# Performance work log

Hardware: AMD Instinct MI355X
Metric: run time of the kernel (lower is better)

Reference implementation:

```python
import jax, jax.numpy as jnp
import numpy as np

H, C_K, C_Q = 4, 512, 512


def setup_inputs() -> dict:
    key = jax.random.key(0)
    ks = jax.random.split(key, 6)
    s = 1.0 / np.sqrt(512.0)
    return {
        "x_k": jax.random.normal(ks[0], (4096, 512), jnp.float32),
        "x_q": jax.random.normal(ks[1], (4096, 512), jnp.float32),
        "k_w": jax.random.normal(ks[2], (H * C_K, 512), jnp.float32) * s,
        "q_w": jax.random.normal(ks[3], (H * C_Q, 512), jnp.float32) * s,
        "attn_w": jax.random.normal(ks[4], (H, C_K, C_Q), jnp.float32) * s,
        "proj_w": jax.random.normal(ks[5], (C_K, C_Q), jnp.float32) * s,
    }


def reference(x_k, x_q, k_w, q_w, attn_w, proj_w):
    # Project keys/queries and split into heads: [H, N, c]
    xk = (x_k @ k_w.T).reshape(-1, H, C_K).transpose(1, 0, 2)
    xq = (x_q @ q_w.T).reshape(-1, H, C_Q).transpose(1, 0, 2)
    # Bilinear scores: alphas[h, n, m] = xk[h,n,:] @ attn_w[h] @ xq[h,m,:]
    alphas = jnp.einsum("hnk,hkq,hmq->hnm", xk, attn_w, xq)
    # key-side update
    alpha_ks = jax.nn.softmax(alphas, axis=2)                 # [H, Nk, Nq]
    alpha_k_agg = jnp.mean(jnp.einsum("hnm,hmq->hnq", alpha_ks, xq), axis=0)
    x_k_update = alpha_k_agg @ proj_w.T                       # [Nk, C_K]
    # query-side update (bidirectional)
    alpha_qs = jax.nn.softmax(alphas.transpose(0, 2, 1), axis=2)  # [H, Nq, Nk]
    alpha_q_agg = jnp.mean(jnp.einsum("hmn,hnk->hmk", alpha_qs, xk), axis=0)
    x_q_update = alpha_q_agg @ proj_w                         # [Nq, C_Q]
    return x_k + x_k_update, x_q + x_q_update
```

## Files before the change

### kernel.cpp

```cpp
#include <hip/hip_runtime.h>
#include <stdint.h>

#define DEVI __device__ __forceinline__

typedef unsigned short u16;
typedef unsigned int u32;
typedef __attribute__((ext_vector_type(4))) unsigned short u16x4;
typedef __attribute__((ext_vector_type(8))) unsigned short u16x8;
typedef __attribute__((ext_vector_type(4))) float f32x4;
typedef __attribute__((ext_vector_type(8))) _Float16 f16x8;

static constexpr int NT = 4096;
static constexpr int D  = 512;
static constexpr int NH = 4;
static constexpr int KS = 4;

DEVI u16 f2h(float f) {
  _Float16 h = (_Float16)f;
  union { _Float16 h; u16 u; } v; v.h = h;
  return v.u;
}
DEVI float h2f(u16 u) {
  union { u16 u; _Float16 h; } v; v.u = u;
  return (float)v.h;
}

DEVI u32 enc_ord(float f) {
  u32 u = __float_as_uint(f);
  return (u & 0x80000000u) ? ~u : (u | 0x80000000u);
}
DEVI float dec_ord(u32 k) {
  u32 u = (k & 0x80000000u) ? (k ^ 0x80000000u) : ~k;
  return __uint_as_float(u);
}

DEVI void gld_lds16(const u16* g, u16* l) {
  __builtin_amdgcn_global_load_lds((const __attribute__((address_space(1))) void*)g,
                                   (__attribute__((address_space(3))) void*)l, 16, 0, 0);
}

enum { OUT_F32 = 0, OUT_F16 = 2, OUT_RES = 3, OUT_SMAX = 4, OUT_F16T = 5 };

template<int OUT>
__global__ __launch_bounds__(256)
void gemm_bt(const u16* __restrict__ A, int lda, size_t zsA,
             const u16* __restrict__ B, int ldb, size_t zsB,
             void* __restrict__ Cp, int ldc, size_t zsC,
             const float* __restrict__ res, const float* __restrict__ res2, int K,
             u32* __restrict__ rmg, u32* __restrict__ cmg,
             u16* __restrict__ STp, int ldct, size_t zsT)
{
  constexpr bool DOT = (OUT == OUT_SMAX || OUT == OUT_F16T);
  __shared__ u16 As[128 * 32];
  __shared__ u16 Bs[128 * 32];
  __shared__ u32 rmaxs[128], cmaxs[128];
  __shared__ u16 Tt[DOT ? 128 * 72 : 8];
  A += blockIdx.z * zsA;
  B += blockIdx.z * zsB;
  const float* resz = (OUT == OUT_RES && blockIdx.z) ? res2 : res;
  const int tid = threadIdx.x;
  const int lane = tid & 63, w = tid >> 6;
  const int wr = w >> 1, wc = w & 1;
  const int m0 = blockIdx.y * 128, n0 = blockIdx.x * 128;

  if (OUT == OUT_SMAX && tid < 128) { rmaxs[tid] = 0u; cmaxs[tid] = 0u; }

  f32x4 acc[4][4] = {};

  for (int k0 = 0; k0 < K; k0 += 32) {
    __syncthreads();
#pragma unroll
    for (int p = 0; p < 2; ++p) {
      int id = p * 256 + tid;
      int row = id >> 2, q = id & 3;
      gld_lds16(A + (size_t)(m0 + row) * lda + k0 + q * 8, As + id * 8);
      gld_lds16(B + (size_t)(n0 + row) * ldb + k0 + q * 8, Bs + id * 8);
    }
    __syncthreads();
    f16x8 af[4], bfv[4];
#pragma unroll
    for (int i = 0; i < 4; ++i)
      af[i] = *(const f16x8*)(As + (wr * 64 + i * 16 + (lane & 15)) * 32 + (lane >> 4) * 8);
#pragma unroll
    for (int i = 0; i < 4; ++i)
      bfv[i] = *(const f16x8*)(Bs + (wc * 64 + i * 16 + (lane & 15)) * 32 + (lane >> 4) * 8);
#pragma unroll
    for (int i = 0; i < 4; ++i)
#pragma unroll
      for (int j = 0; j < 4; ++j)
        acc[i][j] = __builtin_amdgcn_mfma_f32_16x16x32_f16(af[i], bfv[j], acc[i][j], 0, 0, 0);
  }

  if (!DOT) {
#pragma unroll
    for (int i = 0; i < 4; ++i) {
      int rl0 = wr * 64 + i * 16 + (lane >> 4) * 4;
#pragma unroll
      for (int j = 0; j < 4; ++j) {
        int c = n0 + wc * 64 + j * 16 + (lane & 15);
#pragma unroll
        for (int e = 0; e < 4; ++e) {
          size_t idx = blockIdx.z * zsC + (size_t)(m0 + rl0 + e) * ldc + c;
          float v = acc[i][j][e];
          if (OUT == OUT_F32) ((float*)Cp)[idx] = v;
          if (OUT == OUT_F16) ((u16*)Cp)[idx] = f2h(v);
          if (OUT == OUT_RES) ((float*)Cp)[idx] = resz[(size_t)(m0 + rl0 + e) * ldc + c] + v;
        }
      }
    }
  }

  if (OUT == OUT_SMAX) {
#pragma unroll
    for (int i = 0; i < 4; ++i) {
      int rl0 = wr * 64 + i * 16 + (lane >> 4) * 4;
#pragma unroll
      for (int e = 0; e < 4; ++e) {
        float m = fmaxf(fmaxf(acc[i][0][e], acc[i][1][e]), fmaxf(acc[i][2][e], acc[i][3][e]));
        atomicMax(&rmaxs[rl0 + e], enc_ord(m));
      }
    }
#pragma unroll
    for (int j = 0; j < 4; ++j) {
      float m = -3e38f;
#pragma unroll
      for (int i = 0; i < 4; ++i)
#pragma unroll
        for (int e = 0; e < 4; ++e) m = fmaxf(m, acc[i][j][e]);
      atomicMax(&cmaxs[wc * 64 + j * 16 + (lane & 15)], enc_ord(m));
    }
    __syncthreads();
    if (tid < 128) {
      atomicMax(rmg + m0 + tid, rmaxs[tid]);
      atomicMax(cmg + n0 + tid, cmaxs[tid]);
    }
  }

  if (DOT) {
#pragma unroll
    for (int chalf = 0; chalf < 2; ++chalf) {
      __syncthreads();
      if (wc == chalf) {
#pragma unroll
        for (int i = 0; i < 4; ++i) {
          int rl0 = wr * 64 + i * 16 + (lane >> 4) * 4;
#pragma unroll
          for (int j = 0; j < 4; ++j) {
            int c63 = j * 16 + (lane & 15);
#pragma unroll
            for (int e = 0; e < 4; ++e)
              Tt[(rl0 + e) * 72 + c63] = f2h(acc[i][j][e]);
          }
        }
      }
      __syncthreads();
#pragma unroll
      for (int q = 0; q < 4; ++q) {
        int id2 = q * 256 + tid;
        int r = id2 >> 3, c8 = (id2 & 7) * 8;
        u16x8 v = *(const u16x8*)&Tt[r * 72 + c8];
        *(u16x8*)((u16*)Cp + blockIdx.z * zsC + (size_t)(m0 + r) * ldc + n0 + chalf * 64 + c8) = v;
      }
    }
#pragma unroll
    for (int half = 0; half < 2; ++half) {
      __syncthreads();
      if (wr == half) {
#pragma unroll
        for (int i = 0; i < 4; ++i) {
          int rl = i * 16 + (lane >> 4) * 4;
#pragma unroll
          for (int j = 0; j < 4; ++j) {
            int cl = wc * 64 + j * 16 + (lane & 15);
            u16x4 v;
            v[0] = f2h(acc[i][j][0]); v[1] = f2h(acc[i][j][1]);
            v[2] = f2h(acc[i][j][2]); v[3] = f2h(acc[i][j][3]);
            *(u16x4*)&Tt[cl * 72 + rl] = v;
          }
        }
      }
      __syncthreads();
#pragma unroll
      for (int q = 0; q < 4; ++q) {
        int id2 = q * 256 + tid;
        int c = id2 >> 3, mm = (id2 & 7) * 8;
        u16x8 v = *(const u16x8*)&Tt[c * 72 + mm];
        *(u16x8*)(STp + blockIdx.z * zsT + (size_t)(n0 + c) * ldct + m0 + half * 64 + mm) = v;
      }
    }
  }
}

__global__ __launch_bounds__(256)
void pv(const u16* __restrict__ Sarg, const u32* __restrict__ mx_u,
        const u16* __restrict__ B,
        u16* __restrict__ part, float* __restrict__ lpart, int Ksl)
{
  __shared__ u16 As[64 * 40];
  __shared__ u16 Bs[128 * 32];
  __shared__ float ps[4][64];
  const int tid = threadIdx.x;
  const int lane = tid & 63, w = tid >> 6;
  const int wr = w >> 1, wc = w & 1;
  const int m0 = blockIdx.y * 64, n0 = blockIdx.x * 128;
  const int kb = blockIdx.z * Ksl;

  const int rA = tid >> 2, kc = (tid & 3) * 8;
  const float mxA = dec_ord(mx_u[m0 + rA]);
  const u16* S0 = Sarg + (size_t)(m0 + rA) * NT + kb + kc;

  f32x4 acc[2][4] = {};
  float sacc = 0.f;

  f16x8 sv0 = *(const f16x8*)S0;

  for (int k0 = 0; k0 < Ksl; k0 += 32) {
    __syncthreads();
#pragma unroll
    for (int p = 0; p < 2; ++p) {
      int id = p * 256 + tid;
      int row = id >> 2, q = id & 3;
      gld_lds16(B + (size_t)(n0 + row) * NT + kb + k0 + q * 8, Bs + id * 8);
    }
    f16x8 nx0;
    if (k0 + 32 < Ksl) nx0 = *(const f16x8*)(S0 + k0 + 32);
    {
      u16x8 pk;
      float rs = 0.f;
#pragma unroll
      for (int j = 0; j < 8; ++j) {
        float e = __expf((float)sv0[j] - mxA);
        rs += e; pk[j] = f2h(e);
      }
      *(u16x8*)(As + rA * 40 + kc) = pk;
      sacc += rs;
    }
    __syncthreads();
    f16x8 af[2], bfv[4];
#pragma unroll
    for (int i = 0; i < 2; ++i)
      af[i] = *(const f16x8*)(As + (wr * 32 + i * 16 + (lane & 15)) * 40 + (lane >> 4) * 8);
#pragma unroll
    for (int j = 0; j < 4; ++j)
      bfv[j] = *(const f16x8*)(Bs + (wc * 64 + j * 16 + (lane & 15)) * 32 + (lane >> 4) * 8);
#pragma unroll
    for (int i = 0; i < 2; ++i)
#pragma unroll
      for (int j = 0; j < 4; ++j)
        acc[i][j] = __builtin_amdgcn_mfma_f32_16x16x32_f16(af[i], bfv[j], acc[i][j], 0, 0, 0);
    sv0 = nx0;
  }

  u16* out = part + (size_t)blockIdx.z * NT * D;
#pragma unroll
  for (int i = 0; i < 2; ++i) {
    int r0 = m0 + wr * 32 + i * 16 + (lane >> 4) * 4;
#pragma unroll
    for (int j = 0; j < 4; ++j) {
      int c = n0 + wc * 64 + j * 16 + (lane & 15);
#pragma unroll
      for (int e = 0; e < 4; ++e)
        out[(size_t)(r0 + e) * D + c] = f2h(acc[i][j][e]);
    }
  }

  __syncthreads();
  ps[tid & 3][tid >> 2] = sacc;
  __syncthreads();
  if (blockIdx.x == 0 && tid < 64) {
    lpart[(size_t)blockIdx.z * NT + m0 + tid] =
        ps[0][tid] + ps[1][tid] + ps[2][tid] + ps[3][tid];
  }
}

__global__ __launch_bounds__(256)
void reduce2(const u16* __restrict__ pk, const float* __restrict__ lk,
             const u16* __restrict__ pq, const float* __restrict__ lq,
             u16* __restrict__ a0h, u16* __restrict__ a1h)
{
  const size_t i = ((size_t)blockIdx.x * 256 + threadIdx.x) * 4;
  const int m = (int)(i >> 9);
  const size_t zs = (size_t)NT * D;
  float Lk = 0.f, Lq = 0.f;
#pragma unroll
  for (int z = 0; z < KS; ++z) { Lk += lk[(size_t)z * NT + m]; Lq += lq[(size_t)z * NT + m]; }
  float s0 = 0.f, s1 = 0.f, s2 = 0.f, s3 = 0.f;
#pragma unroll
  for (int z = 0; z < KS; ++z) {
    u16x4 v = *(const u16x4*)(pk + z * zs + i);
    s0 += h2f(v[0]); s1 += h2f(v[1]); s2 += h2f(v[2]); s3 += h2f(v[3]);
  }
  float ck = 0.25f / Lk;
  u16x4 a = *(const u16x4*)(a0h + i);
  u16x4 na;
  na[0] = f2h(h2f(a[0]) + s0 * ck); na[1] = f2h(h2f(a[1]) + s1 * ck);
  na[2] = f2h(h2f(a[2]) + s2 * ck); na[3] = f2h(h2f(a[3]) + s3 * ck);
  *(u16x4*)(a0h + i) = na;
  s0 = s1 = s2 = s3 = 0.f;
#pragma unroll
  for (int z = 0; z < KS; ++z) {
    u16x4 v = *(const u16x4*)(pq + z * zs + i);
    s0 += h2f(v[0]); s1 += h2f(v[1]); s2 += h2f(v[2]); s3 += h2f(v[3]);
  }
  float cq = 0.25f / Lq;
  u16x4 b = *(const u16x4*)(a1h + i);
  u16x4 nb;
  nb[0] = f2h(h2f(b[0]) + s0 * cq); nb[1] = f2h(h2f(b[1]) + s1 * cq);
  nb[2] = f2h(h2f(b[2]) + s2 * cq); nb[3] = f2h(h2f(b[3]) + s3 * cq);
  *(u16x4*)(a1h + i) = nb;
}

__global__ __launch_bounds__(256)
void cast_f32_f16(const float* __restrict__ in, u16* __restrict__ out, int n)
{
  int i = (blockIdx.x * 256 + threadIdx.x) * 8;
  if (i >= n) return;
  f32x4 a = *(const f32x4*)(in + i), b = *(const f32x4*)(in + i + 4);
  u16x8 s;
  s[0] = f2h(a[0]); s[1] = f2h(a[1]); s[2] = f2h(a[2]); s[3] = f2h(a[3]);
  s[4] = f2h(b[0]); s[5] = f2h(b[1]); s[6] = f2h(b[2]); s[7] = f2h(b[3]);
  *(u16x8*)(out + i) = s;
}

__global__ __launch_bounds__(256)
void transpose_cast_f32(const float* __restrict__ in, int ldi,
                        u16* __restrict__ out, int ldo)
{
  __shared__ u16 t[64][72];
  int r0 = blockIdx.x * 64, c0 = blockIdx.y * 64;
  int t8 = threadIdx.x & 7, rr = threadIdx.x >> 3;
#pragma unroll
  for (int p = 0; p < 2; ++p) {
    int r = rr + p * 32;
    const float* src = in + (size_t)(r0 + r) * ldi + c0 + t8 * 8;
    f32x4 a = *(const f32x4*)src, b = *(const f32x4*)(src + 4);
    u16x8 s;
    s[0] = f2h(a[0]); s[1] = f2h(a[1]); s[2] = f2h(a[2]); s[3] = f2h(a[3]);
    s[4] = f2h(b[0]); s[5] = f2h(b[1]); s[6] = f2h(b[2]); s[7] = f2h(b[3]);
    *(u16x8*)&t[r][t8 * 8] = s;
  }
  __syncthreads();
#pragma unroll
  for (int p = 0; p < 2; ++p) {
    int c = rr + p * 32;
    u16x8 s;
#pragma unroll
    for (int j = 0; j < 8; ++j) s[j] = t[t8 * 8 + j][c];
    *(u16x8*)(out + (size_t)(c0 + c) * ldo + r0 + t8 * 8) = s;
  }
}

extern "C" void kernel_launch(void* const* d_in, const int* in_sizes, int n_in,
                              void* d_out, int out_size, void* d_ws, size_t ws_size,
                              hipStream_t stream)
{
  const float* x_k    = (const float*)d_in[0];
  const float* x_q    = (const float*)d_in[1];
  const float* k_w    = (const float*)d_in[2];
  const float* q_w    = (const float*)d_in[3];
  const float* attn_w = (const float*)d_in[4];
  const float* proj_w = (const float*)d_in[5];
  float* out0 = (float*)d_out;
  float* out1 = out0 + (size_t)NT * D;

  char* wptr = (char*)d_ws;
  auto alloc = [&](size_t bytes) { char* p = wptr; wptr += (bytes + 255) & ~(size_t)255; return p; };
  u16*   pb     = (u16*)  alloc((size_t)D * D * 2);
  u16*   pbT    = (u16*)  alloc((size_t)D * D * 2);
  u16*   XKall  = (u16*)  alloc((size_t)NT * NH * D * 2);
  u16*   XKTall = (u16*)  alloc((size_t)NT * NH * D * 2);
  u16*   XQTall = (u16*)  alloc((size_t)NT * NH * D * 2);
  u16*   Kpall  = (u16*)  alloc((size_t)NH * NT * D * 2);
  u16*   partK  = (u16*)  alloc((size_t)KS * NT * D * 2);
  u16*   partQ  = (u16*)  alloc((size_t)KS * NT * D * 2);
  u16*   agg0h  = (u16*)  alloc((size_t)NT * D * 2);
  u16*   agg1h  = (u16*)  alloc((size_t)NT * D * 2);
  float* lk     = (float*)alloc((size_t)KS * NT * 4);
  float* lq     = (float*)alloc((size_t)KS * NT * 4);
  u32*   rowm_u = (u32*)  alloc((size_t)NT * 4);
  u32*   colm_u = (u32*)  alloc((size_t)NT * 4);
  u16*   ST     = (u16*)  alloc((size_t)NT * NT * 2);
  char*  Sreg   = alloc((size_t)NT * NT * 2);
  u16*   S      = (u16*)Sreg;
  char* sp = Sreg;
  auto salloc = [&](size_t bytes) { char* p = sp; sp += (bytes + 255) & ~(size_t)255; return p; };
  u16* xkb   = (u16*)salloc((size_t)NT * D * 2);
  u16* xqb   = (u16*)salloc((size_t)NT * D * 2);
  u16* kwb   = (u16*)salloc((size_t)NH * D * D * 2);
  u16* qwb   = (u16*)salloc((size_t)NH * D * D * 2);
  u16* Abf   = (u16*)salloc((size_t)NH * D * D * 2);
  u16* XQall = (u16*)salloc((size_t)NT * NH * D * 2);

  cast_f32_f16<<<NT * D / 2048, 256, 0, stream>>>(x_k, xkb, NT * D);
  cast_f32_f16<<<NT * D / 2048, 256, 0, stream>>>(x_q, xqb, NT * D);
  cast_f32_f16<<<NH * D * D / 2048, 256, 0, stream>>>(k_w, kwb, NH * D * D);
  cast_f32_f16<<<NH * D * D / 2048, 256, 0, stream>>>(q_w, qwb, NH * D * D);
  cast_f32_f16<<<NH * D * D / 2048, 256, 0, stream>>>(attn_w, Abf, NH * D * D);
  cast_f32_f16<<<D * D / 2048, 256, 0, stream>>>(proj_w, pb, D * D);
  transpose_cast_f32<<<dim3(D / 64, D / 64), 256, 0, stream>>>(proj_w, D, pbT, D);

  gemm_bt<OUT_F16T><<<dim3(NH * D / 128, NT / 128, 2), 256, 0, stream>>>(
      xkb, D, (size_t)(xqb - xkb), kwb, D, (size_t)(qwb - kwb),
      XKall, NH * D, (size_t)(XQall - XKall), nullptr, nullptr, D,
      nullptr, nullptr, XKTall, NT, (size_t)(XQTall - XKTall));
  gemm_bt<OUT_F16><<<dim3(D / 128, NT / 128, NH), 256, 0, stream>>>(
      XQall, NH * D, (size_t)D, Abf, D, (size_t)D * D, Kpall, D, (size_t)NT * D,
      nullptr, nullptr, D, nullptr, nullptr, nullptr, 0, 0);

  hipMemsetAsync(agg0h, 0, (size_t)2 * NT * D * 2, stream);

  for (int h = 0; h < NH; ++h) {
    const u16* XKh  = XKall + (size_t)h * D;
    const u16* XKTh = XKTall + (size_t)h * D * NT;
    const u16* XQTh = XQTall + (size_t)h * D * NT;
    const u16* Kph  = Kpall + (size_t)h * NT * D;

    hipMemsetAsync(rowm_u, 0, (size_t)NT * 4 * 2, stream);

    gemm_bt<OUT_SMAX><<<dim3(NT / 128, NT / 128), 256, 0, stream>>>(
        XKh, NH * D, 0, Kph, D, 0, S, NT, 0, nullptr, nullptr, D,
        rowm_u, colm_u, ST, NT, 0);

    pv<<<dim3(D / 128, NT / 64, KS), 256, 0, stream>>>(
        S, rowm_u, XQTh, partK, lk, NT / KS);
    pv<<<dim3(D / 128, NT / 64, KS), 256, 0, stream>>>(
        ST, colm_u, XKTh, partQ, lq, NT / KS);

    reduce2<<<NT * D / 1024, 256, 0, stream>>>(partK, lk, partQ, lq, agg0h, agg1h);
  }

  gemm_bt<OUT_RES><<<dim3(D / 128, NT / 128, 2), 256, 0, stream>>>(
      agg0h, D, (size_t)(agg1h - agg0h), pb, D, (size_t)(pbT - pb),
      out0, D, (size_t)NT * D, x_k, x_q, D, nullptr, nullptr, nullptr, 0, 0);
}
```

Before: 606.3 us.

## Shrink PV tile to 64 columns and write S directly from registers

The PV kernel's output tile goes from 64x128 to 64x64, so each wave computes a 16x64 strip, the grid doubles in x, and the B shared buffer is halved. This raises parallelism and occupancy but doubles the recomputation of exp(S - max) and the reads of S across column blocks. Separately, the DOT/SMAX GEMM now writes the non-transposed S straight from registers with scalar f16 stores, instead of staging it through shared memory for coalesced 16-byte stores. That removes two barriers per half but makes the S writes less coalesced.

```diff
diff --git a/kernel.cpp b/kernel.cpp
--- a/kernel.cpp
+++ b/kernel.cpp
@@ -91,21 +91,19 @@
         acc[i][j] = __builtin_amdgcn_mfma_f32_16x16x32_f16(af[i], bfv[j], acc[i][j], 0, 0, 0);
   }
 
-  if (!DOT) {
-#pragma unroll
-    for (int i = 0; i < 4; ++i) {
-      int rl0 = wr * 64 + i * 16 + (lane >> 4) * 4;
-#pragma unroll
-      for (int j = 0; j < 4; ++j) {
-        int c = n0 + wc * 64 + j * 16 + (lane & 15);
-#pragma unroll
-        for (int e = 0; e < 4; ++e) {
-          size_t idx = blockIdx.z * zsC + (size_t)(m0 + rl0 + e) * ldc + c;
-          float v = acc[i][j][e];
-          if (OUT == OUT_F32) ((float*)Cp)[idx] = v;
-          if (OUT == OUT_F16) ((u16*)Cp)[idx] = f2h(v);
-          if (OUT == OUT_RES) ((float*)Cp)[idx] = resz[(size_t)(m0 + rl0 + e) * ldc + c] + v;
-        }
+#pragma unroll
+  for (int i = 0; i < 4; ++i) {
+    int rl0 = wr * 64 + i * 16 + (lane >> 4) * 4;
+#pragma unroll
+    for (int j = 0; j < 4; ++j) {
+      int c = n0 + wc * 64 + j * 16 + (lane & 15);
+#pragma unroll
+      for (int e = 0; e < 4; ++e) {
+        size_t idx = blockIdx.z * zsC + (size_t)(m0 + rl0 + e) * ldc + c;
+        float v = acc[i][j][e];
+        if (OUT == OUT_F32) ((float*)Cp)[idx] = v;
+        if (OUT == OUT_F16 || DOT) ((u16*)Cp)[idx] = f2h(v);
+        if (OUT == OUT_RES) ((float*)Cp)[idx] = resz[(size_t)(m0 + rl0 + e) * ldc + c] + v;
       }
     }
   }
@@ -137,31 +135,6 @@
   }
 
   if (DOT) {
-#pragma unroll
-    for (int chalf = 0; chalf < 2; ++chalf) {
-      __syncthreads();
-      if (wc == chalf) {
-#pragma unroll
-        for (int i = 0; i < 4; ++i) {
-          int rl0 = wr * 64 + i * 16 + (lane >> 4) * 4;
-#pragma unroll
-          for (int j = 0; j < 4; ++j) {
-            int c63 = j * 16 + (lane & 15);
-#pragma unroll
-            for (int e = 0; e < 4; ++e)
-              Tt[(rl0 + e) * 72 + c63] = f2h(acc[i][j][e]);
-          }
-        }
-      }
-      __syncthreads();
-#pragma unroll
-      for (int q = 0; q < 4; ++q) {
-        int id2 = q * 256 + tid;
-        int r = id2 >> 3, c8 = (id2 & 7) * 8;
-        u16x8 v = *(const u16x8*)&Tt[r * 72 + c8];
-        *(u16x8*)((u16*)Cp + blockIdx.z * zsC + (size_t)(m0 + r) * ldc + n0 + chalf * 64 + c8) = v;
-      }
-    }
 #pragma unroll
     for (int half = 0; half < 2; ++half) {
       __syncthreads();
@@ -197,31 +170,25 @@
         u16* __restrict__ part, float* __restrict__ lpart, int Ksl)
 {
   __shared__ u16 As[64 * 40];
-  __shared__ u16 Bs[128 * 32];
+  __shared__ u16 Bs[64 * 32];
   __shared__ float ps[4][64];
   const int tid = threadIdx.x;
   const int lane = tid & 63, w = tid >> 6;
-  const int wr = w >> 1, wc = w & 1;
-  const int m0 = blockIdx.y * 64, n0 = blockIdx.x * 128;
+  const int m0 = blockIdx.y * 64, n0 = blockIdx.x * 64;
   const int kb = blockIdx.z * Ksl;
 
   const int rA = tid >> 2, kc = (tid & 3) * 8;
   const float mxA = dec_ord(mx_u[m0 + rA]);
   const u16* S0 = Sarg + (size_t)(m0 + rA) * NT + kb + kc;
 
-  f32x4 acc[2][4] = {};
+  f32x4 acc[4] = {};
   float sacc = 0.f;
 
   f16x8 sv0 = *(const f16x8*)S0;
 
   for (int k0 = 0; k0 < Ksl; k0 += 32) {
     __syncthreads();
-#pragma unroll
-    for (int p = 0; p < 2; ++p) {
-      int id = p * 256 + tid;
-      int row = id >> 2, q = id & 3;
-      gld_lds16(B + (size_t)(n0 + row) * NT + kb + k0 + q * 8, Bs + id * 8);
-    }
+    gld_lds16(B + (size_t)(n0 + (tid >> 2)) * NT + kb + k0 + (tid & 3) * 8, Bs + tid * 8);
     f16x8 nx0;
     if (k0 + 32 < Ksl) nx0 = *(const f16x8*)(S0 + k0 + 32);
     {
@@ -236,31 +203,26 @@
       sacc += rs;
     }
     __syncthreads();
-    f16x8 af[2], bfv[4];
-#pragma unroll
-    for (int i = 0; i < 2; ++i)
-      af[i] = *(const f16x8*)(As + (wr * 32 + i * 16 + (lane & 15)) * 40 + (lane >> 4) * 8);
+    f16x8 af, bfv[4];
+    af = *(const f16x8*)(As + (w * 16 + (lane & 15)) * 40 + (lane >> 4) * 8);
 #pragma unroll
     for (int j = 0; j < 4; ++j)
-      bfv[j] = *(const f16x8*)(Bs + (wc * 64 + j * 16 + (lane & 15)) * 32 + (lane >> 4) * 8);
-#pragma unroll
-    for (int i = 0; i < 2; ++i)
-#pragma unroll
-      for (int j = 0; j < 4; ++j)
-        acc[i][j] = __builtin_amdgcn_mfma_f32_16x16x32_f16(af[i], bfv[j], acc[i][j], 0, 0, 0);
+      bfv[j] = *(const f16x8*)(Bs + (j * 16 + (lane & 15)) * 32 + (lane >> 4) * 8);
+#pragma unroll
+    for (int j = 0; j < 4; ++j)
+      acc[j] = __builtin_amdgcn_mfma_f32_16x16x32_f16(af, bfv[j], acc[j], 0, 0, 0);
     sv0 = nx0;
   }
 
   u16* out = part + (size_t)blockIdx.z * NT * D;
-#pragma unroll
-  for (int i = 0; i < 2; ++i) {
-    int r0 = m0 + wr * 32 + i * 16 + (lane >> 4) * 4;
+  {
+    int r0 = m0 + w * 16 + (lane >> 4) * 4;
 #pragma unroll
     for (int j = 0; j < 4; ++j) {
-      int c = n0 + wc * 64 + j * 16 + (lane & 15);
+      int c = n0 + j * 16 + (lane & 15);
 #pragma unroll
       for (int e = 0; e < 4; ++e)
-        out[(size_t)(r0 + e) * D + c] = f2h(acc[i][j][e]);
+        out[(size_t)(r0 + e) * D + c] = f2h(acc[j][e]);
     }
   }
 
@@ -421,9 +383,9 @@
         XKh, NH * D, 0, Kph, D, 0, S, NT, 0, nullptr, nullptr, D,
         rowm_u, colm_u, ST, NT, 0);
 
-    pv<<<dim3(D / 128, NT / 64, KS), 256, 0, stream>>>(
+    pv<<<dim3(D / 64, NT / 64, KS), 256, 0, stream>>>(
         S, rowm_u, XQTh, partK, lk, NT / KS);
-    pv<<<dim3(D / 128, NT / 64, KS), 256, 0, stream>>>(
+    pv<<<dim3(D / 64, NT / 64, KS), 256, 0, stream>>>(
         ST, colm_u, XKTh, partQ, lq, NT / KS);
 
     reduce2<<<NT * D / 1024, 256, 0, stream>>>(partK, lk, partQ, lq, agg0h, agg1h);
```

Result: slower. 803.2 us (+32.5%).
